# Optimization experiments

Measured on AMD Instinct MI355X. Metric: run time of the kernel, lower is better.

## Reference

```python
import jax, jax.numpy as jnp
import numpy as np
from jax import lax

PAD_IDX = 9182


def setup_inputs() -> dict:
    key = jax.random.key(0)
    ks = jax.random.split(key, 16)
    B, S = 16, 256
    V, E, H, SH = 32000, 512, 1024, 1024
    sc = 0.05
    embed = jax.random.normal(ks[0], (V, E), jnp.float32) * sc
    embed = embed.at[PAD_IDX].set(0.0)  # padding_idx row
    inp = {
        "context_encoding": jax.random.normal(ks[1], (B, 1, SH), jnp.float32),
        "target": jax.random.randint(ks[2], (B, S), 0, V),
        "embed": embed,                                              # embed_in.weight (shared out proj)
        "W_s2d": jax.random.normal(ks[3], (H, SH), jnp.float32) * sc,   # ses_to_dec
        "b_s2d": jax.random.normal(ks[4], (H,), jnp.float32) * sc,
        "W_dec_inf": jax.random.normal(ks[5], (2 * E, H), jnp.float32) * sc,
        "W_ses_inf": jax.random.normal(ks[6], (2 * E, SH), jnp.float32) * sc,
        "W_emb_inf": jax.random.normal(ks[7], (2 * E, E), jnp.float32) * sc,
        "b_emb_inf": jax.random.normal(ks[8], (2 * E,), jnp.float32) * sc,
        "W_ih": jax.random.normal(ks[9], (3 * H, E), jnp.float32) * sc,  # GRU input weights
        "W_hh": jax.random.normal(ks[10], (3 * H, H), jnp.float32) * sc,  # GRU hidden weights
        "b_ih": jax.random.normal(ks[11], (3 * H,), jnp.float32) * sc,
        "b_hh": jax.random.normal(ks[12], (3 * H,), jnp.float32) * sc,
    }
    return inp


def _decode(context_encoding, embed, W_s2d, b_s2d, W_dec_inf, W_ses_inf,
            W_emb_inf, b_emb_inf, W_ih, W_hh, b_ih, b_hh, target):
    B, S = target.shape
    ctx = context_encoding[:, 0]                    # [B, SH]
    ses_inf = ctx @ W_ses_inf.T                     # [B, 2E]
    h0 = jnp.tanh(ctx @ W_s2d.T + b_s2d)            # [B, H] init decoder hidden

    emb = embed[target]                             # [B, S, E]
    emb_inf = emb @ W_emb_inf.T + b_emb_inf         # [B, S, 2E]
    x_proj = emb @ W_ih.T + b_ih                    # [B, S, 3H] precomputed GRU input gates

    def gru_step(h, xp):
        gh = h @ W_hh.T + b_hh                      # [B, 3H]
        xr, xz, xn = jnp.split(xp, 3, axis=-1)
        hr, hz, hn = jnp.split(gh, 3, axis=-1)
        r = jax.nn.sigmoid(xr + hr)
        z = jax.nn.sigmoid(xz + hz)
        n = jnp.tanh(xn + r * hn)
        h_new = (1.0 - z) * n + z * h
        return h_new, h_new

    _, hs = lax.scan(gru_step, h0, jnp.swapaxes(x_proj, 0, 1))  # [S, B, H]
    hs = jnp.swapaxes(hs, 0, 1)                     # [B, S, H]

    total = hs @ W_dec_inf.T + ses_inf[:, None, :] + emb_inf  # [B, S, 2E]
    mx = total.reshape(B, S, -1, 2).max(axis=-1)    # maxout pairs -> [B, S, E]
    logits = mx @ embed.T                           # shared embedding out proj [B, S, V]
    return logits


def reference(context_encoding, target, embed, W_s2d, b_s2d, W_dec_inf,
              W_ses_inf, W_emb_inf, b_emb_inf, W_ih, W_hh, b_ih, b_hh):
    dec_o = _decode(context_encoding, embed, W_s2d, b_s2d, W_dec_inf,
                    W_ses_inf, W_emb_inf, b_emb_inf, W_ih, W_hh, b_ih, b_hh,
                    target)
    return dec_o
```

## Files before the change

### kernel.cpp

```cpp
#include <hip/hip_runtime.h>

typedef unsigned short u16;
typedef unsigned int u32;
typedef __attribute__((ext_vector_type(8))) __bf16 bf16x8;
typedef __attribute__((ext_vector_type(4))) float f32x4;
typedef __attribute__((ext_vector_type(4))) u32 u32x4;

#define ASYNC16(g, l) __builtin_amdgcn_global_load_lds( \
    (const __attribute__((address_space(1))) unsigned int*)(g), \
    (__attribute__((address_space(3))) unsigned int*)(l), 16, 0, 0)

__device__ __forceinline__ u16 f2bf(float f){
  unsigned u = __float_as_uint(f);
  unsigned r = u + 0x7fffu + ((u >> 16) & 1u);
  return (u16)(r >> 16);
}

__global__ __launch_bounds__(256) void f2bf_kernel(const float* __restrict__ in,
                                                   u16* __restrict__ out, int n){
  int i = (blockIdx.x * 256 + threadIdx.x) * 8;
  if (i >= n) return;
  float4 a = *(const float4*)&in[i];
  float4 b = *(const float4*)&in[i + 4];
  u16 r[8] = {f2bf(a.x), f2bf(a.y), f2bf(a.z), f2bf(a.w),
              f2bf(b.x), f2bf(b.y), f2bf(b.z), f2bf(b.w)};
  *(uint4*)&out[i] = *(const uint4*)r;
}

__global__ __launch_bounds__(256) void ctx_kernel(const float* __restrict__ ctx,
    const float* __restrict__ Wses, const float* __restrict__ Ws2d,
    const float* __restrict__ bs2d, float* __restrict__ sesinf,
    float* __restrict__ h0f, u16* __restrict__ h0bf){
  int id = blockIdx.x * 4 + (threadIdx.x >> 6);
  int lane = threadIdx.x & 63;
  int n = id & 1023, b = (id >> 10) & 15, mat = id >> 14;
  const float* w = (mat ? Ws2d : Wses) + (size_t)n * 1024;
  const float* x = ctx + (size_t)b * 1024;
  float v = 0.f;
  #pragma unroll 4
  for (int k = lane; k < 1024; k += 64) v += x[k] * w[k];
  #pragma unroll
  for (int off = 32; off; off >>= 1) v += __shfl_down(v, off);
  if (lane == 0){
    if (mat == 0) sesinf[b * 1024 + n] = v;
    else {
      float t = tanhf(v + bs2d[n]);
      h0f[b * 1024 + n] = t;
      h0bf[b * 1024 + n] = f2bf(t);
    }
  }
}

__global__ void gather_kernel(const int* __restrict__ target,
                              const u16* __restrict__ embedBF, u16* __restrict__ embBF){
  int i = blockIdx.x;
  int t = target[i];
  int lane = threadIdx.x;
  *(uint4*)&embBF[(size_t)i * 512 + lane * 8] =
      *(const uint4*)&embedBF[(size_t)t * 512 + lane * 8];
}

template<int EPI, int SWZ>
__global__ __launch_bounds__(256) void gemm_bt(
    const u16* __restrict__ A, const u16* __restrict__ B, float* __restrict__ C,
    int M, int N, int K,
    const float* __restrict__ bias, const float* __restrict__ add0,
    const float* __restrict__ add1, u16* __restrict__ mxout)
{
  __shared__ u16 sA[2][128 * 32];
  __shared__ u16 sB[2][128 * 32];
  int bx = blockIdx.x, by = blockIdx.y;
  if (SWZ){
    int nwg = gridDim.x * gridDim.y;
    int wg = by * gridDim.x + bx;
    int q = nwg >> 3;
    int nw = (wg & 7) * q + (wg >> 3);
    bx = nw % gridDim.x; by = nw / gridDim.x;
  }
  const int n0 = bx * 128;
  const int m0 = by * 128;
  const int tid = threadIdx.x;
  const int lane = tid & 63;
  const int wid = tid >> 6;
  const int wm = (wid >> 1) * 64, wn = (wid & 1) * 64;
  const int l15 = lane & 15, kg = (lane >> 4) * 8;
  (void)M;

  f32x4 zero = {0.f, 0.f, 0.f, 0.f};
  f32x4 acc[4][4];
  #pragma unroll
  for (int m = 0; m < 4; m++)
    #pragma unroll
    for (int n = 0; n < 4; n++) acc[m][n] = zero;

  auto stage = [&](int buf, int kk){
    const u16* Ab = A + (size_t)m0 * K + kk;
    const u16* Bb = B + (size_t)n0 * K + kk;
    #pragma unroll
    for (int j = 0; j < 2; j++){
      int c = j * 256 + tid;
      ASYNC16(Ab + (size_t)(c >> 2) * K + (c & 3) * 8, &sA[buf][c * 8]);
    }
    #pragma unroll
    for (int j = 0; j < 2; j++){
      int c = j * 256 + tid;
      ASYNC16(Bb + (size_t)(c >> 2) * K + (c & 3) * 8, &sB[buf][c * 8]);
    }
  };

  stage(0, 0);
  int cur = 0;
  for (int kk = 0; kk < K; kk += 32){
    __syncthreads();
    if (kk + 32 < K) stage(cur ^ 1, kk + 32);
    bf16x8 af[4], bf_[4];
    #pragma unroll
    for (int m = 0; m < 4; m++)
      af[m] = *(const bf16x8*)&sA[cur][(wm + m * 16 + l15) * 32 + kg];
    #pragma unroll
    for (int n = 0; n < 4; n++)
      bf_[n] = *(const bf16x8*)&sB[cur][(wn + n * 16 + l15) * 32 + kg];
    #pragma unroll
    for (int m = 0; m < 4; m++)
      #pragma unroll
      for (int n = 0; n < 4; n++)
        acc[m][n] = __builtin_amdgcn_mfma_f32_16x16x32_bf16(af[m], bf_[n], acc[m][n], 0, 0, 0);
    cur ^= 1;
  }

  const int rb = m0 + wm + (lane >> 4) * 4;
  const int cb = n0 + wn + l15;
  #pragma unroll
  for (int m = 0; m < 4; m++){
    #pragma unroll
    for (int n = 0; n < 4; n++){
      #pragma unroll
      for (int i = 0; i < 4; i++){
        int row = rb + m * 16 + i;
        int col = cb + n * 16;
        float v = acc[m][n][i];
        if (EPI == 1) v += bias[col];
        if (EPI == 2 || EPI == 3)
          v += add0[(row >> 8) * N + col] + add1[(size_t)row * N + col];
        if (EPI == 3){
          float w = __shfl_xor(v, 1);
          if ((l15 & 1) == 0)
            mxout[(size_t)row * (N >> 1) + (col >> 1)] = f2bf(fmaxf(v, w));
        } else {
          C[(size_t)row * N + col] = v;
        }
      }
    }
  }
}

#define GRU_NWG 64
#define GRU_LDS 145408

__global__ __launch_bounds__(1024) void gru_kernel(
    const u16* __restrict__ WhhBF, const float* __restrict__ bhh,
    const float* __restrict__ xproj, const float* __restrict__ h0f,
    const u16* __restrict__ h0bf, u16* __restrict__ hsBF, int* flags)
{
  extern __shared__ char smem[];
  u16*  Wl   = (u16*)smem;
  u16*  hb   = Wl + 48 * 1032;
  float* gbuf = (float*)(smem + 132096);
  float* hown = gbuf + 12 * 256;

  const int g = blockIdx.x;
  const int j0 = g * 16;
  const int tid = threadIdx.x;
  const int lane = tid & 63;
  const int wid = tid >> 6;
  const int l15 = lane & 15, kh8 = (lane >> 4) * 8;

  for (int c = tid; c < 48 * 128; c += 1024){
    int r = c >> 7, cg = (c & 127) * 8;
    int gate = r >> 4, n = r & 15;
    *(uint4*)&Wl[r * 1032 + cg] =
        *(const uint4*)&WhhBF[(size_t)(gate * 1024 + j0 + n) * 1024 + cg];
  }
  const int bb = (tid & 255) >> 4, jj = tid & 15;
  float bh0 = 0.f, bh1 = 0.f, bh2 = 0.f;
  if (tid < 256){
    hown[bb * 16 + jj] = h0f[bb * 1024 + j0 + jj];
    bh0 = bhh[j0 + jj];
    bh1 = bhh[1024 + j0 + jj];
    bh2 = bhh[2048 + j0 + jj];
  }
  u32* hs32 = (u32*)hsBF;
  __syncthreads();

  for (int s = 0; s < 256; ++s){
    if (s == 0){
      #pragma unroll
      for (int k = 0; k < 2; k++){
        int c = tid + k * 1024;
        int b = c >> 7, cg = (c & 127) * 8;
        *(uint4*)&hb[b * 1032 + cg] = *(const uint4*)&h0bf[b * 1024 + cg];
      }
    } else {
      u32x4 r[2];
      #pragma unroll
      for (int k = 0; k < 2; k++){
        int c = tid + k * 1024;
        int b = c >> 7, cg = (c & 127) * 8;
        const u16* src = &hsBF[(size_t)((b << 8) + s - 1) * 1024 + cg];
        asm volatile("global_load_dwordx4 %0, %1, off sc1"
                     : "=v"(r[k]) : "v"(src) : "memory");
      }
      asm volatile("s_waitcnt vmcnt(0)" ::: "memory");
      __builtin_amdgcn_sched_barrier(0);
      #pragma unroll
      for (int k = 0; k < 2; k++){
        int c = tid + k * 1024;
        int b = c >> 7, cg = (c & 127) * 8;
        *(u32x4*)&hb[b * 1032 + cg] = r[k];
      }
    }

    float xr = 0.f, xz = 0.f, xn = 0.f;
    if (tid < 256){
      const float* xp = xproj + ((size_t)(bb << 8) + s) * 3072;
      xr = xp[j0 + jj]; xz = xp[1024 + j0 + jj]; xn = xp[2048 + j0 + jj];
    }
    __syncthreads();

    if (wid < 12){
      const int gate = wid >> 2, Koff = (wid & 3) * 256;
      f32x4 acc0 = {0.f, 0.f, 0.f, 0.f};
      f32x4 acc1 = {0.f, 0.f, 0.f, 0.f};
      const u16* wrow = &Wl[(gate * 16 + l15) * 1032 + Koff];
      const u16* hrow = &hb[l15 * 1032 + Koff];
      #pragma unroll
      for (int kk = 0; kk < 256; kk += 64){
        bf16x8 a0 = *(const bf16x8*)&hrow[kk + kh8];
        bf16x8 w0 = *(const bf16x8*)&wrow[kk + kh8];
        acc0 = __builtin_amdgcn_mfma_f32_16x16x32_bf16(a0, w0, acc0, 0, 0, 0);
        bf16x8 a1 = *(const bf16x8*)&hrow[kk + 32 + kh8];
        bf16x8 w1 = *(const bf16x8*)&wrow[kk + 32 + kh8];
        acc1 = __builtin_amdgcn_mfma_f32_16x16x32_bf16(a1, w1, acc1, 0, 0, 0);
      }
      #pragma unroll
      for (int i = 0; i < 4; ++i)
        gbuf[wid * 256 + ((lane >> 4) * 4 + i) * 16 + l15] = acc0[i] + acc1[i];
    }
    __syncthreads();

    if (tid < 256){
      int ic = bb * 16 + jj;
      float hr = gbuf[0 * 256 + ic] + gbuf[1 * 256 + ic] +
                 gbuf[2 * 256 + ic] + gbuf[3 * 256 + ic] + bh0;
      float hz = gbuf[4 * 256 + ic] + gbuf[5 * 256 + ic] +
                 gbuf[6 * 256 + ic] + gbuf[7 * 256 + ic] + bh1;
      float hn = gbuf[8 * 256 + ic] + gbuf[9 * 256 + ic] +
                 gbuf[10 * 256 + ic] + gbuf[11 * 256 + ic] + bh2;
      float r = 1.f / (1.f + __expf(-(xr + hr)));
      float z = 1.f / (1.f + __expf(-(xz + hz)));
      float nn = tanhf(xn + r * hn);
      float hnew = (1.f - z) * nn + z * hown[bb * 16 + jj];
      hown[bb * 16 + jj] = hnew;
      float hnext = __shfl_down(hnew, 1);
      if ((jj & 1) == 0){
        u32 pack = (u32)f2bf(hnew) | ((u32)f2bf(hnext) << 16);
        size_t e = (size_t)((bb << 8) + s) * 1024 + j0 + jj;
        __hip_atomic_store(&hs32[e >> 1], pack, __ATOMIC_RELAXED,
                           __HIP_MEMORY_SCOPE_AGENT);
      }
    }

    if (s < 255){
      asm volatile("s_waitcnt vmcnt(0)" ::: "memory");
      __syncthreads();
      if (tid == 0)
        __hip_atomic_store(&flags[g * 32], s + 1, __ATOMIC_RELAXED,
                           __HIP_MEMORY_SCOPE_AGENT);
      if (wid == 0){
        while (__hip_atomic_load(&flags[lane * 32], __ATOMIC_RELAXED,
                                 __HIP_MEMORY_SCOPE_AGENT) <= s)
          __builtin_amdgcn_s_sleep(1);
      }
      __syncthreads();
    }
  }
}

extern "C" void kernel_launch(void* const* d_in, const int* in_sizes, int n_in,
                              void* d_out, int out_size, void* d_ws, size_t ws_size,
                              hipStream_t stream)
{
  const float* ctx    = (const float*)d_in[0];
  const int*   target = (const int*)d_in[1];
  const float* embed  = (const float*)d_in[2];
  const float* Ws2d   = (const float*)d_in[3];
  const float* bs2d   = (const float*)d_in[4];
  const float* Wdec   = (const float*)d_in[5];
  const float* Wses   = (const float*)d_in[6];
  const float* Wemb   = (const float*)d_in[7];
  const float* bemb   = (const float*)d_in[8];
  const float* Wih    = (const float*)d_in[9];
  const float* Whh    = (const float*)d_in[10];
  const float* bih    = (const float*)d_in[11];
  const float* bhh    = (const float*)d_in[12];
  float* out = (float*)d_out;

  char* ws = (char*)d_ws;
  size_t off = 0;
  auto alloc = [&](size_t bytes)->char*{
    char* p = ws + off; off += (bytes + 255) & ~(size_t)255; return p;
  };
  u16*   embedBF = (u16*)alloc(32000ull * 512 * 2);
  u16*   WihBF   = (u16*)alloc(3072ull * 512 * 2);
  u16*   WembBF  = (u16*)alloc(1024ull * 512 * 2);
  u16*   WdecBF  = (u16*)alloc(1024ull * 1024 * 2);
  u16*   WhhBF   = (u16*)alloc(3072ull * 1024 * 2);
  u16*   embBF   = (u16*)alloc(4096ull * 512 * 2);
  float* xproj   = (float*)alloc(4096ull * 3072 * 4);
  float* embinf  = (float*)alloc(4096ull * 1024 * 4);
  float* sesinf  = (float*)alloc(16ull * 1024 * 4);
  float* h0f     = (float*)alloc(16ull * 1024 * 4);
  u16*   h0bf    = (u16*)alloc(16ull * 1024 * 2);
  u16*   hsBF    = (u16*)alloc(4096ull * 1024 * 2);
  u16*   mxBF    = (u16*)alloc(4096ull * 512 * 2);
  int*   flags   = (int*)alloc(16384);
  (void)ws_size; (void)in_sizes; (void)n_in; (void)out_size;

  hipFuncSetAttribute((const void*)gru_kernel,
                      hipFuncAttributeMaxDynamicSharedMemorySize, GRU_LDS);
  hipMemsetAsync(flags, 0, 16384, stream);

  auto conv = [&](const float* in, u16* o, size_t n){
    f2bf_kernel<<<dim3((unsigned)((n / 8 + 255) / 256)), 256, 0, stream>>>(in, o, (int)n);
  };
  conv(embed, embedBF, 32000ull * 512);
  conv(Wih,   WihBF,   3072ull * 512);
  conv(Wemb,  WembBF,  1024ull * 512);
  conv(Wdec,  WdecBF,  1024ull * 1024);
  conv(Whh,   WhhBF,   3072ull * 1024);

  ctx_kernel<<<8192, 256, 0, stream>>>(ctx, Wses, Ws2d, bs2d, sesinf, h0f, h0bf);
  gather_kernel<<<4096, 64, 0, stream>>>(target, embedBF, embBF);

  gemm_bt<1,0><<<dim3(3072 / 128, 4096 / 128), 256, 0, stream>>>(
      embBF, WihBF, xproj, 4096, 3072, 512, bih, nullptr, nullptr, nullptr);
  gemm_bt<1,0><<<dim3(1024 / 128, 4096 / 128), 256, 0, stream>>>(
      embBF, WembBF, embinf, 4096, 1024, 512, bemb, nullptr, nullptr, nullptr);

  gru_kernel<<<GRU_NWG, 1024, GRU_LDS, stream>>>(WhhBF, bhh, xproj, h0f, h0bf, hsBF, flags);

  gemm_bt<3,0><<<dim3(1024 / 128, 4096 / 128), 256, 0, stream>>>(
      hsBF, WdecBF, nullptr, 4096, 1024, 1024, nullptr, sesinf, embinf, mxBF);

  gemm_bt<0,1><<<dim3(32000 / 128, 4096 / 128), 256, 0, stream>>>(
      mxBF, embedBF, out, 4096, 32000, 512, nullptr, nullptr, nullptr, nullptr);
}
```

Measured before the change: 1.159 ms.

## Replace GRU per-step flag barrier with step-tagged hidden-state exchange buffer

The per-step inter-workgroup barrier (flag store plus spin on all 64 flags) is replaced by a double-buffered exchange array where each hidden value is stored packed with its step number. Consumers poll their own slice until every tag matches the current step, so synchronisation is per datum instead of a global barrier. This removes the barrier round trip and its extra syncthreads, but doubles the bytes read per step, adds tag checking and retry loops, and writes hs as scattered 16-bit stores.

```diff
diff --git a/kernel.cpp b/kernel.cpp
--- a/kernel.cpp
+++ b/kernel.cpp
@@ -160,7 +160,7 @@
 __global__ __launch_bounds__(1024) void gru_kernel(
     const u16* __restrict__ WhhBF, const float* __restrict__ bhh,
     const float* __restrict__ xproj, const float* __restrict__ h0f,
-    const u16* __restrict__ h0bf, u16* __restrict__ hsBF, int* flags)
+    const u16* __restrict__ h0bf, u16* __restrict__ hsBF, u32* __restrict__ xb)
 {
   extern __shared__ char smem[];
   u16*  Wl   = (u16*)smem;
@@ -189,34 +189,66 @@
     bh1 = bhh[1024 + j0 + jj];
     bh2 = bhh[2048 + j0 + jj];
   }
-  u32* hs32 = (u32*)hsBF;
+  const int c0 = tid,         b0 = c0 >> 7, cg0 = (c0 & 127) * 8;
+  const int c1 = tid + 1024,  b1 = c1 >> 7, cg1 = (c1 & 127) * 8;
   __syncthreads();
 
   for (int s = 0; s < 256; ++s){
     if (s == 0){
-      #pragma unroll
-      for (int k = 0; k < 2; k++){
-        int c = tid + k * 1024;
-        int b = c >> 7, cg = (c & 127) * 8;
-        *(uint4*)&hb[b * 1032 + cg] = *(const uint4*)&h0bf[b * 1024 + cg];
-      }
+      *(uint4*)&hb[b0 * 1032 + cg0] = *(const uint4*)&h0bf[b0 * 1024 + cg0];
+      *(uint4*)&hb[b1 * 1032 + cg1] = *(const uint4*)&h0bf[b1 * 1024 + cg1];
     } else {
-      u32x4 r[2];
-      #pragma unroll
-      for (int k = 0; k < 2; k++){
-        int c = tid + k * 1024;
-        int b = c >> 7, cg = (c & 127) * 8;
-        const u16* src = &hsBF[(size_t)((b << 8) + s - 1) * 1024 + cg];
-        asm volatile("global_load_dwordx4 %0, %1, off sc1"
-                     : "=v"(r[k]) : "v"(src) : "memory");
-      }
-      asm volatile("s_waitcnt vmcnt(0)" ::: "memory");
-      __builtin_amdgcn_sched_barrier(0);
-      #pragma unroll
-      for (int k = 0; k < 2; k++){
-        int c = tid + k * 1024;
-        int b = c >> 7, cg = (c & 127) * 8;
-        *(u32x4*)&hb[b * 1032 + cg] = r[k];
+      const u32* base = xb + ((u32)(s & 1) << 14);
+      const u32* p0 = base + b0 * 1024 + cg0;
+      const u32* p1 = base + b1 * 1024 + cg1;
+      u32 need = 3u;
+      u32x4 ta, tb, tc, td;
+      while (need){
+        if (need & 1u){
+          asm volatile("global_load_dwordx4 %0, %1, off sc1"
+                       : "=v"(ta) : "v"(p0) : "memory");
+          asm volatile("global_load_dwordx4 %0, %1, off sc1"
+                       : "=v"(tb) : "v"(p0 + 4) : "memory");
+        }
+        if (need & 2u){
+          asm volatile("global_load_dwordx4 %0, %1, off sc1"
+                       : "=v"(tc) : "v"(p1) : "memory");
+          asm volatile("global_load_dwordx4 %0, %1, off sc1"
+                       : "=v"(td) : "v"(p1 + 4) : "memory");
+        }
+        asm volatile("s_waitcnt vmcnt(0)" ::: "memory");
+        __builtin_amdgcn_sched_barrier(0);
+        if (need & 1u){
+          u32 m = ((ta[0] ^ (u32)s) | (ta[1] ^ (u32)s) |
+                   (ta[2] ^ (u32)s) | (ta[3] ^ (u32)s) |
+                   (tb[0] ^ (u32)s) | (tb[1] ^ (u32)s) |
+                   (tb[2] ^ (u32)s) | (tb[3] ^ (u32)s)) & 0xFFFFu;
+          if (m == 0){
+            u32 dd[4];
+            dd[0] = __builtin_amdgcn_perm(ta[1], ta[0], 0x07060302u);
+            dd[1] = __builtin_amdgcn_perm(ta[3], ta[2], 0x07060302u);
+            dd[2] = __builtin_amdgcn_perm(tb[1], tb[0], 0x07060302u);
+            dd[3] = __builtin_amdgcn_perm(tb[3], tb[2], 0x07060302u);
+            *(uint4*)&hb[b0 * 1032 + cg0] = *(const uint4*)dd;
+            need &= ~1u;
+          }
+        }
+        if (need & 2u){
+          u32 m = ((tc[0] ^ (u32)s) | (tc[1] ^ (u32)s) |
+                   (tc[2] ^ (u32)s) | (tc[3] ^ (u32)s) |
+                   (td[0] ^ (u32)s) | (td[1] ^ (u32)s) |
+                   (td[2] ^ (u32)s) | (td[3] ^ (u32)s)) & 0xFFFFu;
+          if (m == 0){
+            u32 dd[4];
+            dd[0] = __builtin_amdgcn_perm(tc[1], tc[0], 0x07060302u);
+            dd[1] = __builtin_amdgcn_perm(tc[3], tc[2], 0x07060302u);
+            dd[2] = __builtin_amdgcn_perm(td[1], td[0], 0x07060302u);
+            dd[3] = __builtin_amdgcn_perm(td[3], td[2], 0x07060302u);
+            *(uint4*)&hb[b1 * 1032 + cg1] = *(const uint4*)dd;
+            need &= ~2u;
+          }
+        }
+        if (need) __builtin_amdgcn_s_sleep(1);
       }
     }
 
@@ -261,27 +293,13 @@
       float nn = tanhf(xn + r * hn);
       float hnew = (1.f - z) * nn + z * hown[bb * 16 + jj];
       hown[bb * 16 + jj] = hnew;
-      float hnext = __shfl_down(hnew, 1);
-      if ((jj & 1) == 0){
-        u32 pack = (u32)f2bf(hnew) | ((u32)f2bf(hnext) << 16);
-        size_t e = (size_t)((bb << 8) + s) * 1024 + j0 + jj;
-        __hip_atomic_store(&hs32[e >> 1], pack, __ATOMIC_RELAXED,
-                           __HIP_MEMORY_SCOPE_AGENT);
+      u16 hv = f2bf(hnew);
+      hsBF[((size_t)(bb << 8) + s) * 1024 + j0 + jj] = hv;
+      if (s < 255){
+        u32 pack = ((u32)hv << 16) | (u32)(s + 1);
+        __hip_atomic_store(&xb[((u32)(((s + 1) & 1)) << 14) + bb * 1024 + j0 + jj],
+                           pack, __ATOMIC_RELAXED, __HIP_MEMORY_SCOPE_AGENT);
       }
-    }
-
-    if (s < 255){
-      asm volatile("s_waitcnt vmcnt(0)" ::: "memory");
-      __syncthreads();
-      if (tid == 0)
-        __hip_atomic_store(&flags[g * 32], s + 1, __ATOMIC_RELAXED,
-                           __HIP_MEMORY_SCOPE_AGENT);
-      if (wid == 0){
-        while (__hip_atomic_load(&flags[lane * 32], __ATOMIC_RELAXED,
-                                 __HIP_MEMORY_SCOPE_AGENT) <= s)
-          __builtin_amdgcn_s_sleep(1);
-      }
-      __syncthreads();
     }
   }
 }
@@ -323,12 +341,12 @@
   u16*   h0bf    = (u16*)alloc(16ull * 1024 * 2);
   u16*   hsBF    = (u16*)alloc(4096ull * 1024 * 2);
   u16*   mxBF    = (u16*)alloc(4096ull * 512 * 2);
-  int*   flags   = (int*)alloc(16384);
+  u32*   xbuf    = (u32*)alloc(2ull * 16 * 1024 * 4);
   (void)ws_size; (void)in_sizes; (void)n_in; (void)out_size;
 
   hipFuncSetAttribute((const void*)gru_kernel,
                       hipFuncAttributeMaxDynamicSharedMemorySize, GRU_LDS);
-  hipMemsetAsync(flags, 0, 16384, stream);
+  hipMemsetAsync(xbuf, 0, 2ull * 16 * 1024 * 4, stream);
 
   auto conv = [&](const float* in, u16* o, size_t n){
     f2bf_kernel<<<dim3((unsigned)((n / 8 + 255) / 256)), 256, 0, stream>>>(in, o, (int)n);
@@ -347,7 +365,8 @@
   gemm_bt<1,0><<<dim3(1024 / 128, 4096 / 128), 256, 0, stream>>>(
       embBF, WembBF, embinf, 4096, 1024, 512, bemb, nullptr, nullptr, nullptr);
 
-  gru_kernel<<<GRU_NWG, 1024, GRU_LDS, stream>>>(WhhBF, bhh, xproj, h0f, h0bf, hsBF, flags);
+  gru_kernel<<<GRU_NWG, 1024, GRU_LDS, stream>>>(WhhBF, bhh, xproj, h0f, h0bf,
+                                                 hsBF, xbuf);
 
   gemm_bt<3,0><<<dim3(1024 / 128, 4096 / 128), 256, 0, stream>>>(
       hsBF, WdecBF, nullptr, 4096, 1024, 1024, nullptr, sesinf, embinf, mxBF);
```

Measured after the change: 1.389 ms. 1.2x slower.
